# Kernel optimization log

Hardware: AMD Instinct MI355X
Metric: run time of the kernel (lower is better)

## Reference

```python
import jax, jax.numpy as jnp
import numpy as np

PI = 3.141592653589793
TAU = 0.5          # gumbel-softmax temperature
EPS = 1e-6
B, N, D = 128, 32, 256

def _linear(x, w, b=None):
    y = x @ w.T
    return y if b is None else y + b

def _wrap(a):
    return (a + PI) % (2 * PI) - PI

def setup_inputs() -> dict:
    key = jax.random.key(0)
    ks = jax.random.split(key, 16)
    s = 0.05
    return {
        "embedding": jax.random.normal(ks[0], (B, N, 11), jnp.float32),
        "gumbel_u": jax.random.uniform(ks[1], (B * N, N - 1, 2), jnp.float32),
        "emb1_w": jax.random.normal(ks[2], (128, 5), jnp.float32) * s,
        "emb1_b": jnp.zeros((128,), jnp.float32),
        "emb2_w": jax.random.normal(ks[3], (D, 128), jnp.float32) * s,
        "emb2_b": jnp.zeros((D,), jnp.float32),
        "hm1_w": jax.random.normal(ks[4], (D, D + 7), jnp.float32) * s,
        "hm1_b": jnp.zeros((D,), jnp.float32),
        "hm2_w": jax.random.normal(ks[5], (D, D), jnp.float32) * s,
        "hm2_b": jnp.zeros((D,), jnp.float32),
        "he_w": jax.random.normal(ks[6], (2, D), jnp.float32) * s,
        "he_b": jnp.zeros((2,), jnp.float32),
        "q_w": jax.random.normal(ks[7], (D, D), jnp.float32) * s,
        "k_w": jax.random.normal(ks[8], (D, 10), jnp.float32) * s,
        "v_w": jax.random.normal(ks[9], (D, 10), jnp.float32) * s,
        "v_b": jnp.zeros((D,), jnp.float32),
        "dec_w": jax.random.normal(ks[10], (2 * D, 2 * D), jnp.float32) * s,
        "dec_b": jnp.zeros((2 * D,), jnp.float32),
    }

def reference(embedding, gumbel_u, emb1_w, emb1_b, emb2_w, emb2_b,
              hm1_w, hm1_b, hm2_w, hm2_b, he_w, he_b,
              q_w, k_w, v_w, v_b, dec_w, dec_b):
    b, n, _ = embedding.shape
    d = q_w.shape[0]
    # static off-diagonal index lists (i,j), j != i, row-major like mask indexing
    rows, cols = np.nonzero(~np.eye(n, dtype=bool))

    embed = embedding[:, :, 4:9].reshape(b * n, 5)
    position = embedding[:, :, :2]
    heading = embedding[:, :, 2:4]
    action = embedding[:, :, 7:9]
    goal = embedding[:, :, -2:]

    # agent embedding MLP (leaky_relu slope 0.01, torch default)
    h = jax.nn.leaky_relu(_linear(embed, emb1_w, emb1_b))
    agent_embed = jax.nn.leaky_relu(_linear(h, emb2_w, emb2_b)).reshape(b, n, d)

    # pairwise geometry  [b,i,j,...]
    rel_vec = position[:, None, :, :] - position[:, :, None, :]   # pos_j - pos_i
    dx, dy = rel_vec[..., 0], rel_vec[..., 1]
    rel_dist = jnp.linalg.norm(rel_vec, axis=-1, keepdims=True) / 12.0
    heading_angle_i = jnp.arctan2(heading[..., 1], heading[..., 0])[:, :, None]  # [b,n,1]
    angle = _wrap(jnp.arctan2(dy, dx) - heading_angle_i)
    hj_cos = jnp.broadcast_to(heading[:, None, :, 0], (b, n, n))
    hj_sin = jnp.broadcast_to(heading[:, None, :, 1], (b, n, n))
    action_j = jnp.broadcast_to(action[:, None, :, :], (b, n, n, 2))
    edge_features = jnp.concatenate([
        rel_dist, jnp.cos(angle)[..., None], jnp.sin(angle)[..., None],
        hj_cos[..., None], hj_sin[..., None], action_j], axis=-1)  # [b,n,n,7]

    # hard attention branch (off-diagonal pairs only)
    h_i_flat = jnp.broadcast_to(agent_embed[:, :, None, :], (b, n, n - 1, d)).reshape(b * n, n - 1, d)
    edge_flat = edge_features[:, rows, cols].reshape(b * n, n - 1, 7)
    hard_input = jnp.concatenate([h_i_flat, edge_flat], axis=-1)
    h_hard = _linear(jax.nn.relu(_linear(hard_input, hm1_w, hm1_b)), hm2_w, hm2_b)
    hard_logits = _linear(h_hard, he_w, he_b)                      # [b*n, n-1, 2]
    g = -jnp.log(-jnp.log(gumbel_u + 1e-10) + 1e-10)
    hard_soft = jax.nn.softmax((hard_logits + g) / TAU, axis=-1)
    hard_weights = hard_soft[..., 1].reshape(b, n, n - 1)

    unnorm = jnp.linalg.norm(rel_vec, axis=-1, keepdims=True)      # [b,n,n,1]
    unnorm_rel_dist = unnorm[:, rows, cols].reshape(b * n, n - 1, 1)

    # goal polar features
    goal_rel_vec = goal[:, None, :, :] - position[:, :, None, :]   # [b,n,n,2]
    goal_rel_dist = jnp.linalg.norm(goal_rel_vec, axis=-1, keepdims=True)
    goal_rel_angle = _wrap(jnp.arctan2(goal_rel_vec[..., 1], goal_rel_vec[..., 0]) - heading_angle_i)
    goal_polar = jnp.concatenate([goal_rel_dist, jnp.cos(goal_rel_angle)[..., None],
                                  jnp.sin(goal_rel_angle)[..., None]], axis=-1)
    soft_edge = jnp.concatenate([edge_features, goal_polar], axis=-1)  # [b,n,n,10]

    # soft attention (vectorized over agents; off-diagonal gather)
    q = agent_embed @ q_w.T                                         # [b,n,d]
    k = soft_edge @ k_w.T                                           # [b,n,n,d]
    v = jax.nn.relu(_linear(soft_edge, v_w, v_b))                   # [b,n,n,d]
    k_off = k[:, rows, cols].reshape(b, n, n - 1, d)
    v_off = v[:, rows, cols].reshape(b, n, n - 1, d)
    score = jnp.einsum('bnd,bnjd->bnj', q, k_off) / jnp.sqrt(jnp.float32(d))
    soft_w = jax.nn.softmax(score, axis=-1)
    combined = soft_w * hard_weights                                # [b,n,n-1]
    x = jnp.einsum('bnjd,bnj->bnd', v_off, combined).reshape(b * n, d)

    final_input = jnp.concatenate([agent_embed.reshape(b * n, d), x], axis=-1)
    output = _linear(final_input, dec_w, dec_b)                     # [b*n, 2d]

    cwn = combined / (combined.sum(axis=-1, keepdims=True) + EPS)
    mean_entropy = (-(cwn * jnp.log(cwn + EPS)).sum(axis=-1)).mean()
    comb_w = combined.reshape(n, -1)  # matches torch.stack(dim=1).reshape(n, -1)

    return (output, hard_logits[..., 1], unnorm_rel_dist, mean_entropy, hard_weights, comb_w)
```

## Files before the change

### kernel.cpp

```cpp
#include <hip/hip_runtime.h>
#include <hip/hip_bf16.h>
#include <math.h>

typedef __hip_bfloat16 bf16;
typedef short bf16x8 __attribute__((ext_vector_type(8)));
typedef float f32x4 __attribute__((ext_vector_type(4)));
typedef unsigned short u16;

#define R_TOT 4096
#define NJ 31

#define OFF_AE   0
#define OFF_QK   1048576
#define OFF_S1   2097152
#define OFF_ENT  4542464
#define OFF_X    4546560
#define OFF_W    5595136
#define W_E1W   0
#define W_E1B   640
#define W_E2P   768
#define W_E2B   33536
#define W_H1B   101120
#define W_W1EP  167684
#define W_HE2P  171780
#define W_CB    173828
#define W_S1P   200452
#define W_VW    235780
#define W_VB    238340
#define W_DECWT 238596
#define W_DECB  500740
#define W_QKM   501252

#define OUT0 0
#define OUT1 2097152
#define OUT2 2224128
#define OUT3 2351104
#define OUT4 2351105
#define OUT5 2478081

__device__ __forceinline__ float b2f(bf16 x) { return __bfloat162float(x); }
__device__ __forceinline__ float ldin(const void* p, int i, int flag) {
    return flag ? b2f(((const bf16*)p)[i]) : ((const float*)p)[i];
}
__device__ __forceinline__ void stout(void* p, int i, float v, int flag) {
    if (flag) ((bf16*)p)[i] = __float2bfloat16(v);
    else      ((float*)p)[i] = v;
}
__device__ __forceinline__ u16 f2bbits(float v) {
    bf16 h = __float2bfloat16(v);
    return *(u16*)&h;
}
__device__ __forceinline__ int detect_flag(const void* emb) {
    float x = ((const float*)emb)[threadIdx.x & 63];
    int sane = (x == x) && (fabsf(x) < 1e20f);
    unsigned long long m = __ballot(sane);
    return (__popcll(m) == 64) ? 0 : 1;
}

__global__ __launch_bounds__(256) void k_prep(
        const void* emb,
        const void* e1w, const void* e1b, const void* e2w, const void* e2b,
        const void* h1w, const void* h1b, const void* qw,  const void* kw,
        const void* vw,  const void* vb,  const void* decb,
        float* W) {
    int flag = detect_flag(emb);
    int blk = blockIdx.x;
    int tid = threadIdx.x;
    if (blk < 384) {
        int p; const void* src; int ldm, Wdst;
        if (blk < 128) { p = blk * 256 + tid;         src = e2w; ldm = 128; Wdst = W_E2P; }
        else           { p = (blk - 128) * 256 + tid; src = h1w; ldm = 263; Wdst = W_S1P; }
        int jj   = p & 7;
        int lane = (p >> 3) & 63;
        int tile = p >> 9;
        int nt = tile & 15, kt = tile >> 4;
        int n = nt * 16 + (lane & 15);
        int k = kt * 32 + ((lane >> 4) << 3) + jj;
        ((u16*)(W + Wdst))[p] = f2bbits(ldin(src, n * ldm + k, flag));
    } else if (blk < 640) {
        int p = (blk - 384) * 16 + (tid >> 4);
        int l = tid & 15;
        int jj = p & 7, lane = (p >> 3) & 63, kt = p >> 9;
        int k = kt * 32 + ((lane >> 4) << 3) + jj;
        int n = lane & 15;
        float v = 0.f;
        if (n < 10) {
#pragma unroll
            for (int dd = 0; dd < 16; dd++) {
                int d = l + 16 * dd;
                v += ldin(qw, d * 256 + k, flag) * ldin(kw, d * 10 + n, flag);
            }
        }
        v += __shfl_xor(v, 1, 64); v += __shfl_xor(v, 2, 64);
        v += __shfl_xor(v, 4, 64); v += __shfl_xor(v, 8, 64);
        if (l == 0) ((u16*)(W + W_QKM))[p] = f2bbits(v);
    } else {
        int q2 = (blk - 640) * 256 + tid;
        if      (q2 < 640)   W[W_E1W  + q2]           = ldin(e1w,  q2,          flag);
        else if (q2 < 768)   W[W_E1B  + (q2 - 640)]   = ldin(e1b,  q2 - 640,    flag);
        else if (q2 < 1024)  W[W_E2B  + (q2 - 768)]   = ldin(e2b,  q2 - 768,    flag);
        else if (q2 < 1280)  W[W_H1B  + (q2 - 1024)]  = ldin(h1b,  q2 - 1024,   flag);
        else if (q2 < 3840)  W[W_VW   + (q2 - 1280)]  = ldin(vw,   q2 - 1280,   flag);
        else if (q2 < 4096)  W[W_VB   + (q2 - 3840)]  = ldin(vb,   q2 - 3840,   flag);
        else if (q2 < 4608)  W[W_DECB + (q2 - 4096)]  = ldin(decb, q2 - 4096,   flag);
    }
}

__global__ __launch_bounds__(256) void k_embed(const void* emb, const float* W_,
                                               const void* h1w, const void* h2w, const void* h2b,
                                               const void* hew, const void* heb, const void* decw,
                                               u16* aeb, float* qkws, float* s1ws) {
    int flag = detect_flag(emb);
    float* W = (float*)W_;
    int blk = blockIdx.x;
    int tid = threadIdx.x;
    if (blk >= 256) {
        if (blk < 1280) {
            int idx = (blk - 256) * 256 + tid;
            int jj   = idx & 7;
            int lane = (idx >> 3) & 63;
            int tile = idx >> 9;
            int nt = tile & 31, kt = tile >> 5;
            int n = nt * 16 + (lane & 15);
            int k = kt * 32 + ((lane >> 4) << 3) + jj;
            ((u16*)(W + W_DECWT))[idx] = f2bbits(ldin(decw, n * 512 + k, flag));
        } else if (blk < 1312) {
            int p = (blk - 1280) * 256 + tid;
            int jj = p & 7, lane = (p >> 3) & 63, nt = p >> 9;
            int n = nt * 16 + (lane & 15);
            int k = ((lane >> 4) << 3) + jj;
            float v = (k < 7) ? ldin(h1w, n * 263 + 256 + k, flag) : 0.f;
            ((u16*)(W + W_W1EP))[p] = f2bbits(v);
        } else if (blk < 1568) {
            int q = (blk - 1312) * 16 + (tid >> 4);
            int l = tid & 15;
            int jj = q & 7, lane = (q >> 3) & 63, kt = q >> 9;
            int n = lane & 15;
            int c = kt * 32 + ((lane >> 4) << 3) + jj;
            float v = 0.f;
            if (n < 2) {
#pragma unroll
                for (int dd = 0; dd < 16; dd++) {
                    int d = l + 16 * dd;
                    v += ldin(hew, n * 256 + d, flag) * ldin(h2w, d * 256 + c, flag);
                }
            }
            v += __shfl_xor(v, 1, 64); v += __shfl_xor(v, 2, 64);
            v += __shfl_xor(v, 4, 64); v += __shfl_xor(v, 8, 64);
            if (l == 0) ((u16*)(W + W_HE2P))[q] = f2bbits(v);
        } else {
            if (tid < 32) {
                int i = tid >> 4, l = tid & 15;
                float v = 0.f;
#pragma unroll
                for (int dd = 0; dd < 16; dd++) {
                    int d = l + 16 * dd;
                    v += ldin(hew, i * 256 + d, flag) * ldin(h2b, d, flag);
                }
                v += __shfl_xor(v, 1, 64); v += __shfl_xor(v, 2, 64);
                v += __shfl_xor(v, 4, 64); v += __shfl_xor(v, 8, 64);
                if (l == 0) W[W_CB + i] = v + ldin(heb, i, flag);
            }
        }
        return;
    }
    int r0 = blk * 16;
    __shared__ float embL[16][12];
    __shared__ u16 hB[16][136];
    __shared__ u16 aeB[16][264];
    for (int idx = tid; idx < 16 * 11; idx += 256) {
        int s = idx / 11, t = idx % 11;
        embL[s][t] = ldin(emb, (r0 + s) * 11 + t, flag);
    }
    __syncthreads();
    for (int idx = tid; idx < 16 * 128; idx += 256) {
        int s = idx >> 7, jo = idx & 127;
        float v = W[W_E1B + jo];
#pragma unroll
        for (int t = 0; t < 5; t++) v += W[W_E1W + jo * 5 + t] * embL[s][4 + t];
        hB[s][jo] = f2bbits(v > 0.f ? v : 0.01f * v);
    }
    __syncthreads();
    int wv = tid >> 6, ln = tid & 63;
    int lr = ln & 15, quad = ln >> 4;
    {
        const bf16x8* Bp = (const bf16x8*)(W + W_E2P);
        f32x4 acc[4];
#pragma unroll
        for (int nt = 0; nt < 4; nt++) acc[nt] = (f32x4){0.f, 0.f, 0.f, 0.f};
#pragma unroll
        for (int kt = 0; kt < 4; kt++) {
            bf16x8 af = *(const bf16x8*)&hB[lr][kt * 32 + (quad << 3)];
#pragma unroll
            for (int nt = 0; nt < 4; nt++) {
                bf16x8 bfr = Bp[(kt * 16 + (wv * 4 + nt)) * 64 + ln];
                acc[nt] = __builtin_amdgcn_mfma_f32_16x16x32_bf16(af, bfr, acc[nt], 0, 0, 0);
            }
        }
#pragma unroll
        for (int nt = 0; nt < 4; nt++) {
            int d = wv * 64 + nt * 16 + lr;
            float bias = W[W_E2B + d];
#pragma unroll
            for (int reg = 0; reg < 4; reg++) {
                int m = quad * 4 + reg;
                float v = acc[nt][reg] + bias;
                v = v > 0.f ? v : 0.01f * v;
                u16 bits = f2bbits(v);
                aeB[m][d] = bits;
                aeb[(r0 + m) * 256 + d] = bits;
            }
        }
    }
    __syncthreads();
    {
        const bf16x8* Bs = (const bf16x8*)(W + W_S1P);
        f32x4 sac[4];
#pragma unroll
        for (int nt = 0; nt < 4; nt++) sac[nt] = (f32x4){0.f, 0.f, 0.f, 0.f};
#pragma unroll
        for (int kt = 0; kt < 8; kt++) {
            bf16x8 af = *(const bf16x8*)&aeB[lr][kt * 32 + (quad << 3)];
#pragma unroll
            for (int nt = 0; nt < 4; nt++) {
                bf16x8 bs = Bs[(kt * 16 + (wv * 4 + nt)) * 64 + ln];
                sac[nt] = __builtin_amdgcn_mfma_f32_16x16x32_bf16(af, bs, sac[nt], 0, 0, 0);
            }
        }
#pragma unroll
        for (int nt = 0; nt < 4; nt++) {
            int d = wv * 64 + nt * 16 + lr;
            float bias = W[W_H1B + d];
#pragma unroll
            for (int reg = 0; reg < 4; reg++) {
                int m = quad * 4 + reg;
                s1ws[(r0 + m) * 256 + d] = sac[nt][reg] + bias;
            }
        }
        if (wv == 0) {
            const bf16x8* Bm = (const bf16x8*)(W + W_QKM);
            f32x4 qk = (f32x4){0.f, 0.f, 0.f, 0.f};
#pragma unroll
            for (int kt = 0; kt < 8; kt++) {
                bf16x8 af = *(const bf16x8*)&aeB[lr][kt * 32 + (quad << 3)];
                qk = __builtin_amdgcn_mfma_f32_16x16x32_bf16(af, Bm[kt * 64 + ln], qk, 0, 0, 0);
            }
            if (lr < 10) {
#pragma unroll
                for (int reg = 0; reg < 4; reg++) {
                    int m = quad * 4 + reg;
                    qkws[(r0 + m) * 10 + lr] = qk[reg];
                }
            }
        }
    }
}

__global__ __launch_bounds__(256) void k_fused(const void* emb, const void* gum,
                                               const float* s1ws, const float* qkws, const float* W,
                                               u16* xb, float* entws, void* out) {
    int flag = detect_flag(emb);
    int r = blockIdx.x;
    int b = r >> 5, i = r & 31;
    __shared__ float embB[32][12];
    __shared__ float seL[32][10];
    __shared__ u16 eA[32][32];
    __shared__ u16 a1[32][264];
    __shared__ float pj[4][32][2];
    __shared__ float cL[32];
    __shared__ float qkL[10];
    int tid = threadIdx.x;
    for (int idx = tid; idx < 32 * 11; idx += 256) {
        int s = idx / 11, t = idx % 11;
        embB[s][t] = ldin(emb, (b * 32 + s) * 11 + t, flag);
    }
    for (int idx = tid; idx < 32 * 32; idx += 256) ((u16*)eA)[idx] = 0;
    if (tid >= 64 && tid < 74) qkL[tid - 64] = qkws[r * 10 + (tid - 64)];
    __syncthreads();
    if (tid < NJ) {
        int jp = tid;
        int j = jp + (jp >= i ? 1 : 0);
        float pix = embB[i][0], piy = embB[i][1], hix = embB[i][2], hiy = embB[i][3];
        float pjx = embB[j][0], pjy = embB[j][1], hjx = embB[j][2], hjy = embB[j][3];
        float ajx = embB[j][7], ajy = embB[j][8];
        float gjx = embB[j][9], gjy = embB[j][10];
        float dx = pjx - pix, dy = pjy - piy;
        float dist = sqrtf(dx * dx + dy * dy);
        float hai = atan2f(hiy, hix);
        float ang = atan2f(dy, dx) - hai;
        float gx = gjx - pix, gy = gjy - piy;
        float gdist = sqrtf(gx * gx + gy * gy);
        float gang = atan2f(gy, gx) - hai;
        float f[10];
        f[0] = dist * (1.f / 12.f);
        f[1] = cosf(ang); f[2] = sinf(ang);
        f[3] = hjx; f[4] = hjy; f[5] = ajx; f[6] = ajy;
        f[7] = gdist; f[8] = cosf(gang); f[9] = sinf(gang);
#pragma unroll
        for (int t = 0; t < 10; t++) seL[jp][t] = f[t];
#pragma unroll
        for (int t = 0; t < 7; t++) eA[jp][t] = f2bbits(f[t]);
        stout(out, OUT2 + r * NJ + jp, dist, flag);
    }
    __syncthreads();
    int wv = tid >> 6, ln = tid & 63;
    int lr = ln & 15, quad = ln >> 4;
    {
        const bf16x8* Bp = (const bf16x8*)(W + W_W1EP);
        bf16x8 af0 = *(const bf16x8*)&eA[lr][quad << 3];
        bf16x8 af1 = *(const bf16x8*)&eA[16 + lr][quad << 3];
#pragma unroll
        for (int nt = 0; nt < 4; nt++) {
            int gnt = wv * 4 + nt;
            int d = gnt * 16 + lr;
            float s1v = s1ws[r * 256 + d];
            f32x4 acc0 = (f32x4){s1v, s1v, s1v, s1v};
            f32x4 acc1 = acc0;
            bf16x8 bb = Bp[gnt * 64 + ln];
            acc0 = __builtin_amdgcn_mfma_f32_16x16x32_bf16(af0, bb, acc0, 0, 0, 0);
            acc1 = __builtin_amdgcn_mfma_f32_16x16x32_bf16(af1, bb, acc1, 0, 0, 0);
#pragma unroll
            for (int reg = 0; reg < 4; reg++) {
                a1[(quad << 2) + reg][d]      = f2bbits(fmaxf(acc0[reg], 0.f));
                a1[16 + (quad << 2) + reg][d] = f2bbits(fmaxf(acc1[reg], 0.f));
            }
        }
    }
    __syncthreads();
    {
        const bf16x8* Ep = (const bf16x8*)(W + W_HE2P);
        f32x4 l0 = (f32x4){0.f, 0.f, 0.f, 0.f};
        f32x4 l1 = (f32x4){0.f, 0.f, 0.f, 0.f};
#pragma unroll
        for (int kk = 0; kk < 2; kk++) {
            int kt = wv * 2 + kk;
            bf16x8 a0 = *(const bf16x8*)&a1[lr][kt * 32 + (quad << 3)];
            bf16x8 a1f = *(const bf16x8*)&a1[16 + lr][kt * 32 + (quad << 3)];
            bf16x8 bb = Ep[kt * 64 + ln];
            l0 = __builtin_amdgcn_mfma_f32_16x16x32_bf16(a0, bb, l0, 0, 0, 0);
            l1 = __builtin_amdgcn_mfma_f32_16x16x32_bf16(a1f, bb, l1, 0, 0, 0);
        }
        if (lr < 2) {
#pragma unroll
            for (int reg = 0; reg < 4; reg++) {
                pj[wv][(quad << 2) + reg][lr]      = l0[reg];
                pj[wv][16 + (quad << 2) + reg][lr] = l1[reg];
            }
        }
    }
    __syncthreads();
    if (wv == 0) {
        float hwv = 0.f;
        if (ln < NJ) {
            float p0 = pj[0][ln][0] + pj[1][ln][0] + pj[2][ln][0] + pj[3][ln][0];
            float p1 = pj[0][ln][1] + pj[1][ln][1] + pj[2][ln][1] + pj[3][ln][1];
            float l0 = p0 + W[W_CB + 0], l1 = p1 + W[W_CB + 1];
            float u0 = ldin(gum, (r * NJ + ln) * 2 + 0, flag);
            float u1 = ldin(gum, (r * NJ + ln) * 2 + 1, flag);
            float g0 = -logf(-logf(u0 + 1e-10f) + 1e-10f);
            float g1 = -logf(-logf(u1 + 1e-10f) + 1e-10f);
            float dl = ((l1 + g1) - (l0 + g0)) * 2.0f;
            hwv = 1.f / (1.f + expf(-dl));
            stout(out, OUT1 + r * NJ + ln, l1, flag);
            stout(out, OUT4 + r * NJ + ln, hwv, flag);
        }
        float sc = -1e30f;
        if (ln < NJ) {
            float p = 0.f;
#pragma unroll
            for (int t = 0; t < 10; t++) p += qkL[t] * seL[ln][t];
            sc = p * (1.f / 16.f);
        }
        float m = sc;
#pragma unroll
        for (int s = 32; s >= 1; s >>= 1) m = fmaxf(m, __shfl_xor(m, s, 64));
        float e = (ln < NJ) ? expf(sc - m) : 0.f;
        float sum = e;
#pragma unroll
        for (int s = 32; s >= 1; s >>= 1) sum += __shfl_xor(sum, s, 64);
        float sw = e / sum;
        float cmb = sw * hwv;
        if (ln < NJ) {
            cL[ln] = cmb;
            stout(out, OUT5 + r * NJ + ln, cmb, flag);
        }
        float csum = cmb;
#pragma unroll
        for (int s = 32; s >= 1; s >>= 1) csum += __shfl_xor(csum, s, 64);
        float cwn = cmb / (csum + 1e-6f);
        float et = (ln < NJ) ? -cwn * logf(cwn + 1e-6f) : 0.f;
#pragma unroll
        for (int s = 32; s >= 1; s >>= 1) et += __shfl_xor(et, s, 64);
        if (ln == 0) entws[r] = et;
    }
    __syncthreads();
    float vwr[10];
#pragma unroll
    for (int t = 0; t < 10; t++) vwr[t] = W[W_VW + tid * 10 + t];
    float vbv = W[W_VB + tid];
    float x = 0.f;
    for (int j = 0; j < NJ; j++) {
        float v = vbv;
#pragma unroll
        for (int t = 0; t < 10; t++) v += vwr[t] * seL[j][t];
        v = fmaxf(v, 0.f);
        x += v * cL[j];
    }
    xb[r * 256 + tid] = f2bbits(x);
}

__global__ __launch_bounds__(256) void k_dec(const void* emb, const u16* aeb, const u16* xb,
                                             const float* W, const float* entws, void* out) {
    int flag = detect_flag(emb);
    int r0 = (blockIdx.x >> 2) * 32;
    int nq = blockIdx.x & 3;
    __shared__ u16 finB[32][520];
    int tid = threadIdx.x;
    for (int idx = tid; idx < 32 * 512; idx += 256) {
        int s = idx >> 9, c = idx & 511;
        finB[s][c] = (c < 256) ? aeb[(r0 + s) * 256 + c] : xb[(r0 + s) * 256 + (c - 256)];
    }
    __syncthreads();
    int wv = tid >> 6, ln = tid & 63;
    int lr = ln & 15, quad = ln >> 4;
    const bf16x8* Bp = (const bf16x8*)(W + W_DECWT);
    f32x4 acc[2][2];
#pragma unroll
    for (int mt = 0; mt < 2; mt++)
#pragma unroll
        for (int nt = 0; nt < 2; nt++) acc[mt][nt] = (f32x4){0.f, 0.f, 0.f, 0.f};
#pragma unroll
    for (int kt = 0; kt < 16; kt++) {
        bf16x8 af[2];
#pragma unroll
        for (int mt = 0; mt < 2; mt++)
            af[mt] = *(const bf16x8*)&finB[mt * 16 + lr][kt * 32 + (quad << 3)];
#pragma unroll
        for (int nt = 0; nt < 2; nt++) {
            int gnt = nq * 8 + wv * 2 + nt;
            bf16x8 bfr = Bp[(kt * 32 + gnt) * 64 + ln];
#pragma unroll
            for (int mt = 0; mt < 2; mt++)
                acc[mt][nt] = __builtin_amdgcn_mfma_f32_16x16x32_bf16(af[mt], bfr, acc[mt][nt], 0, 0, 0);
        }
    }
#pragma unroll
    for (int nt = 0; nt < 2; nt++) {
        int d = (nq * 8 + wv * 2 + nt) * 16 + lr;
        float bias = W[W_DECB + d];
#pragma unroll
        for (int mt = 0; mt < 2; mt++)
#pragma unroll
            for (int reg = 0; reg < 4; reg++) {
                int m = mt * 16 + quad * 4 + reg;
                stout(out, OUT0 + (r0 + m) * 512 + d, acc[mt][nt][reg] + bias, flag);
            }
    }
    if (blockIdx.x == 0) {
        __shared__ float red[4];
        float s = 0.f;
        for (int i2 = tid; i2 < R_TOT; i2 += 256) s += entws[i2];
#pragma unroll
        for (int m = 32; m >= 1; m >>= 1) s += __shfl_xor(s, m, 64);
        if ((tid & 63) == 0) red[tid >> 6] = s;
        __syncthreads();
        if (tid == 0) {
            float t = red[0] + red[1] + red[2] + red[3];
            stout(out, OUT3, t / (float)R_TOT, flag);
        }
    }
}

extern "C" void kernel_launch(void* const* d_in, const int* in_sizes, int n_in,
                              void* d_out, int out_size, void* d_ws, size_t ws_size,
                              hipStream_t stream) {
    const void* emb  = d_in[0];
    const void* gum  = d_in[1];
    const void* e1w  = d_in[2];
    const void* e1b  = d_in[3];
    const void* e2w  = d_in[4];
    const void* e2b  = d_in[5];
    const void* h1w  = d_in[6];
    const void* h1b  = d_in[7];
    const void* h2w  = d_in[8];
    const void* h2b  = d_in[9];
    const void* hew  = d_in[10];
    const void* heb  = d_in[11];
    const void* qw   = d_in[12];
    const void* kw   = d_in[13];
    const void* vw   = d_in[14];
    const void* vb   = d_in[15];
    const void* decw = d_in[16];
    const void* decb = d_in[17];

    float* wsf = (float*)d_ws;
    u16*   aeb  = (u16*)(wsf + OFF_AE);
    float* qkws = wsf + OFF_QK;
    float* s1ws = wsf + OFF_S1;
    float* entw = wsf + OFF_ENT;
    u16*   xb   = (u16*)(wsf + OFF_X);
    float* W    = wsf + OFF_W;

    hipLaunchKernelGGL(k_prep, dim3(659), dim3(256), 0, stream,
                       emb, e1w, e1b, e2w, e2b, h1w, h1b, qw, kw, vw, vb, decb, W);
    hipLaunchKernelGGL(k_embed, dim3(1569), dim3(256), 0, stream,
                       emb, W, h1w, h2w, h2b, hew, heb, decw, aeb, qkws, s1ws);
    hipLaunchKernelGGL(k_fused, dim3(4096), dim3(256), 0, stream,
                       emb, gum, s1ws, qkws, W, xb, entw, d_out);
    hipLaunchKernelGGL(k_dec, dim3(512), dim3(256), 0, stream, emb, aeb, xb, W, entw, d_out);
}
```

Baseline: 155.2 us.

## Replace trig with rsqrt rotation identities and compute V projection via MFMA

The per-pair geometry drops atan2/cos/sin and gets the relative-angle cos and sin from normalized vectors with rotation identities, using rsqrt. The V projection (soft_edge @ v_w) moves from a scalar 31x10 loop per thread to bf16 MFMA tiles that reuse the A fragments already loaded for the hm1 product. A packed bf16 copy of v_w is built in extra k_embed blocks. V values are now computed in bf16 instead of fp32, which costs some accuracy, and zero-vector edge cases are handled explicitly.

```diff
diff --git a/kernel.cpp b/kernel.cpp
--- a/kernel.cpp
+++ b/kernel.cpp
@@ -21,6 +21,7 @@
 #define W_E2P   768
 #define W_E2B   33536
 #define W_H1B   101120
+#define W_VWP   101376
 #define W_W1EP  167684
 #define W_HE2P  171780
 #define W_CB    173828
@@ -109,6 +110,7 @@
 __global__ __launch_bounds__(256) void k_embed(const void* emb, const float* W_,
                                                const void* h1w, const void* h2w, const void* h2b,
                                                const void* hew, const void* heb, const void* decw,
+                                               const void* vw,
                                                u16* aeb, float* qkws, float* s1ws) {
     int flag = detect_flag(emb);
     float* W = (float*)W_;
@@ -148,7 +150,7 @@
             v += __shfl_xor(v, 1, 64); v += __shfl_xor(v, 2, 64);
             v += __shfl_xor(v, 4, 64); v += __shfl_xor(v, 8, 64);
             if (l == 0) ((u16*)(W + W_HE2P))[q] = f2bbits(v);
-        } else {
+        } else if (blk == 1568) {
             if (tid < 32) {
                 int i = tid >> 4, l = tid & 15;
                 float v = 0.f;
@@ -161,6 +163,13 @@
                 v += __shfl_xor(v, 4, 64); v += __shfl_xor(v, 8, 64);
                 if (l == 0) W[W_CB + i] = v + ldin(heb, i, flag);
             }
+        } else {
+            int p = (blk - 1569) * 256 + tid;
+            int jj = p & 7, lane = (p >> 3) & 63, nt = p >> 9;
+            int n = nt * 16 + (lane & 15);
+            int k = ((lane >> 4) << 3) + jj;
+            float v = (k < 10) ? ldin(vw, n * 10 + k, flag) : 0.f;
+            ((u16*)(W + W_VWP))[p] = f2bbits(v);
         }
         return;
     }
@@ -264,7 +273,7 @@
     int b = r >> 5, i = r & 31;
     __shared__ float embB[32][12];
     __shared__ float seL[32][10];
-    __shared__ u16 eA[32][32];
+    __shared__ u16 eA[32][40];
     __shared__ u16 a1[32][264];
     __shared__ float pj[4][32][2];
     __shared__ float cL[32];
@@ -274,7 +283,7 @@
         int s = idx / 11, t = idx % 11;
         embB[s][t] = ldin(emb, (b * 32 + s) * 11 + t, flag);
     }
-    for (int idx = tid; idx < 32 * 32; idx += 256) ((u16*)eA)[idx] = 0;
+    for (int idx = tid; idx < 32 * 40; idx += 256) ((u16*)eA)[idx] = 0;
     if (tid >= 64 && tid < 74) qkL[tid - 64] = qkws[r * 10 + (tid - 64)];
     __syncthreads();
     if (tid < NJ) {
@@ -284,31 +293,41 @@
         float pjx = embB[j][0], pjy = embB[j][1], hjx = embB[j][2], hjy = embB[j][3];
         float ajx = embB[j][7], ajy = embB[j][8];
         float gjx = embB[j][9], gjy = embB[j][10];
+        float hn2 = hix * hix + hiy * hiy;
+        float csh, snh;
+        if (hn2 == 0.f) { csh = 1.f; snh = 0.f; }
+        else { float invh = rsqrtf(hn2); csh = hix * invh; snh = hiy * invh; }
         float dx = pjx - pix, dy = pjy - piy;
-        float dist = sqrtf(dx * dx + dy * dy);
-        float hai = atan2f(hiy, hix);
-        float ang = atan2f(dy, dx) - hai;
+        float d2 = dx * dx + dy * dy;
+        float dist, csd, snd;
+        if (d2 == 0.f) { dist = 0.f; csd = 1.f; snd = 0.f; }
+        else { float invd = rsqrtf(d2); dist = d2 * invd; csd = dx * invd; snd = dy * invd; }
         float gx = gjx - pix, gy = gjy - piy;
-        float gdist = sqrtf(gx * gx + gy * gy);
-        float gang = atan2f(gy, gx) - hai;
+        float g2 = gx * gx + gy * gy;
+        float gdist, csg, sng;
+        if (g2 == 0.f) { gdist = 0.f; csg = 1.f; sng = 0.f; }
+        else { float invg = rsqrtf(g2); gdist = g2 * invg; csg = gx * invg; sng = gy * invg; }
         float f[10];
         f[0] = dist * (1.f / 12.f);
-        f[1] = cosf(ang); f[2] = sinf(ang);
+        f[1] = csd * csh + snd * snh;
+        f[2] = snd * csh - csd * snh;
         f[3] = hjx; f[4] = hjy; f[5] = ajx; f[6] = ajy;
-        f[7] = gdist; f[8] = cosf(gang); f[9] = sinf(gang);
-#pragma unroll
-        for (int t = 0; t < 10; t++) seL[jp][t] = f[t];
-#pragma unroll
-        for (int t = 0; t < 7; t++) eA[jp][t] = f2bbits(f[t]);
+        f[7] = gdist;
+        f[8] = csg * csh + sng * snh;
+        f[9] = sng * csh - csg * snh;
+#pragma unroll
+        for (int t = 0; t < 10; t++) { seL[jp][t] = f[t]; eA[jp][t] = f2bbits(f[t]); }
         stout(out, OUT2 + r * NJ + jp, dist, flag);
     }
     __syncthreads();
     int wv = tid >> 6, ln = tid & 63;
     int lr = ln & 15, quad = ln >> 4;
+    bf16x8 af0 = *(const bf16x8*)&eA[lr][quad << 3];
+    bf16x8 af1 = *(const bf16x8*)&eA[16 + lr][quad << 3];
+    f32x4 vacc[2][4];
     {
         const bf16x8* Bp = (const bf16x8*)(W + W_W1EP);
-        bf16x8 af0 = *(const bf16x8*)&eA[lr][quad << 3];
-        bf16x8 af1 = *(const bf16x8*)&eA[16 + lr][quad << 3];
+        const bf16x8* Bv = (const bf16x8*)(W + W_VWP);
 #pragma unroll
         for (int nt = 0; nt < 4; nt++) {
             int gnt = wv * 4 + nt;
@@ -324,6 +343,10 @@
                 a1[(quad << 2) + reg][d]      = f2bbits(fmaxf(acc0[reg], 0.f));
                 a1[16 + (quad << 2) + reg][d] = f2bbits(fmaxf(acc1[reg], 0.f));
             }
+            bf16x8 bv = Bv[gnt * 64 + ln];
+            f32x4 z = (f32x4){0.f, 0.f, 0.f, 0.f};
+            vacc[0][nt] = __builtin_amdgcn_mfma_f32_16x16x32_bf16(af0, bv, z, 0, 0, 0);
+            vacc[1][nt] = __builtin_amdgcn_mfma_f32_16x16x32_bf16(af1, bv, z, 0, 0, 0);
         }
     }
     __syncthreads();
@@ -350,6 +373,7 @@
     }
     __syncthreads();
     if (wv == 0) {
+        if (ln == 31) cL[31] = 0.f;
         float hwv = 0.f;
         if (ln < NJ) {
             float p0 = pj[0][ln][0] + pj[1][ln][0] + pj[2][ln][0] + pj[3][ln][0];
@@ -394,19 +418,27 @@
         if (ln == 0) entws[r] = et;
     }
     __syncthreads();
-    float vwr[10];
-#pragma unroll
-    for (int t = 0; t < 10; t++) vwr[t] = W[W_VW + tid * 10 + t];
-    float vbv = W[W_VB + tid];
-    float x = 0.f;
-    for (int j = 0; j < NJ; j++) {
-        float v = vbv;
-#pragma unroll
-        for (int t = 0; t < 10; t++) v += vwr[t] * seL[j][t];
-        v = fmaxf(v, 0.f);
-        x += v * cL[j];
-    }
-    xb[r * 256 + tid] = f2bbits(x);
+    {
+        float cj[2][4];
+#pragma unroll
+        for (int mt = 0; mt < 2; mt++)
+#pragma unroll
+            for (int reg = 0; reg < 4; reg++) cj[mt][reg] = cL[mt * 16 + (quad << 2) + reg];
+#pragma unroll
+        for (int nt = 0; nt < 4; nt++) {
+            int d = (wv * 4 + nt) * 16 + lr;
+            float vb = W[W_VB + d];
+            float xp = 0.f;
+#pragma unroll
+            for (int mt = 0; mt < 2; mt++)
+#pragma unroll
+                for (int reg = 0; reg < 4; reg++)
+                    xp += fmaxf(vacc[mt][nt][reg] + vb, 0.f) * cj[mt][reg];
+            xp += __shfl_xor(xp, 16, 64);
+            xp += __shfl_xor(xp, 32, 64);
+            if (quad == 0) xb[r * 256 + d] = f2bbits(xp);
+        }
+    }
 }
 
 __global__ __launch_bounds__(256) void k_dec(const void* emb, const u16* aeb, const u16* xb,
@@ -503,8 +535,8 @@
 
     hipLaunchKernelGGL(k_prep, dim3(659), dim3(256), 0, stream,
                        emb, e1w, e1b, e2w, e2b, h1w, h1b, qw, kw, vw, vb, decb, W);
-    hipLaunchKernelGGL(k_embed, dim3(1569), dim3(256), 0, stream,
-                       emb, W, h1w, h2w, h2b, hew, heb, decw, aeb, qkws, s1ws);
+    hipLaunchKernelGGL(k_embed, dim3(1601), dim3(256), 0, stream,
+                       emb, W, h1w, h2w, h2b, hew, heb, decw, vw, aeb, qkws, s1ws);
     hipLaunchKernelGGL(k_fused, dim3(4096), dim3(256), 0, stream,
                        emb, gum, s1ws, qkws, W, xb, entw, d_out);
     hipLaunchKernelGGL(k_dec, dim3(512), dim3(256), 0, stream, emb, aeb, xb, W, entw, d_out);
```

New measurement: 152.8 us, median of 2. About the same (-1.5%).
